# Performance work log

Measured on AMD Instinct MI355X. Metric: run time of the kernel, lower is better.

## Reference

```python
import math
import jax, jax.numpy as jnp
import numpy as np

B, L, D = 8, 512, 32
SEQ_LEN = 512.0
N_PATCHES, N_REF = 16, 32
LAT, HM = 128, 4
FH, NL, FF = 8, 3, 128
PRED = 96

def _time_embed(t, d):
    # interleaved sin/cos embedding, matching PositionalEmbedding's div_term
    div = jnp.exp(jnp.arange(0, d, 2, dtype=jnp.float32) * (-math.log(10000.0) / d))
    ang = t[..., None] * div
    out = jnp.zeros(t.shape + (d,), dtype=jnp.float32)
    return out.at[..., 0::2].set(jnp.sin(ang)).at[..., 1::2].set(jnp.cos(ang))

def _layernorm(x, g, b):
    mu = jnp.mean(x, axis=-1, keepdims=True)
    var = jnp.var(x, axis=-1, keepdims=True)
    return (x - mu) / jnp.sqrt(var + 1e-5) * g + b

def _mha(z, Wq, Wk, Wv, Wo, bq, bk, bv, bo):
    N, S, dm = z.shape
    hd = dm // FH
    q = (z @ Wq + bq).reshape(N, S, FH, hd)
    k = (z @ Wk + bk).reshape(N, S, FH, hd)
    v = (z @ Wv + bv).reshape(N, S, FH, hd)
    s = jnp.einsum('nqhe,nkhe->nhqk', q, k) / math.sqrt(hd)
    a = jax.nn.softmax(s, axis=-1)
    o = jnp.einsum('nhqk,nkhe->nqhe', a, v).reshape(N, S, dm)
    return o @ Wo + bo

def _forward(x, x_mark, x_mask, Wq, Wk, W_out, b_out, f_Wq, f_Wk, f_Wv, f_Wo, f_bq, f_bk, f_bv, f_bo, f_ln1_g, f_ln1_b, f_W1, f_b1, f_W2, f_b2, f_ln2_g, f_ln2_b, ln_f_g, ln_f_b, W_lin, b_lin):
    t = x_mark[:, :, 0]                                   # [B, L] irregular timestamps in [0, SEQ_LEN]
    edges = jnp.linspace(0.0, SEQ_LEN, N_PATCHES + 1)
    refs = jnp.linspace(0.0, SEQ_LEN, N_REF * N_PATCHES).reshape(N_PATCHES, N_REF)
    obs_valid = jnp.sum(x_mask, axis=-1) > 0              # [B, L]
    dk = LAT // HM
    Kmat = (_time_embed(t, LAT) @ Wk).reshape(B, L, HM, dk)
    v = x * x_mask                                        # mask values like `v = v * m` in original
    reprs = []
    for i in range(N_PATCHES):  # fixed small structural loop
        # _split_patch equivalent: per-channel masked attention is permutation
        # invariant, so the sort/scatter compaction reduces to masking.
        in_patch = (t >= edges[i]) & (t <= edges[i + 1]) & obs_valid   # [B, L]
        Qi = (_time_embed(refs[i], LAT) @ Wq).reshape(N_REF, HM, dk)
        scores = jnp.einsum('rhe,blhe->bhrl', Qi, Kmat) / math.sqrt(dk)
        cmask = x_mask * in_patch[..., None].astype(x.dtype)           # [B, L, D]
        neg = jnp.where(cmask[:, None, None, :, :] > 0, 0.0, -1e9)     # [B,1,1,L,D]
        p = jax.nn.softmax(scores[..., None] + neg, axis=3)            # [B,H,R,L,D]
        attn = jnp.einsum('bhrld,bld->brhd', p, v)                     # [B,R,H,D]
        reprs.append(attn.reshape(B, N_REF, HM * D) @ W_out + b_out)   # [B,R,D]
    rp = jnp.stack(reprs, axis=1)                          # [B, NP, R, D]
    z = rp.transpose(0, 3, 1, 2).reshape(B * D, N_PATCHES, N_REF)
    z = z + _time_embed(jnp.arange(N_PATCHES, dtype=jnp.float32), N_REF)[None]
    for l in range(NL):
        a = _mha(z, f_Wq[l], f_Wk[l], f_Wv[l], f_Wo[l], f_bq[l], f_bk[l], f_bv[l], f_bo[l])
        z = _layernorm(z + a, f_ln1_g[l], f_ln1_b[l])
        y = jax.nn.gelu(z @ f_W1[l] + f_b1[l]) @ f_W2[l] + f_b2[l]
        z = _layernorm(z + y, f_ln2_g[l], f_ln2_b[l])
    z = _layernorm(z, ln_f_g, ln_f_b)
    emb = z.reshape(B, D, N_PATCHES, N_REF).transpose(0, 1, 3, 2)      # [B, D, R, NP]
    out = emb.reshape(B, D, N_REF * N_PATCHES) @ W_lin + b_lin         # [B, D, PRED]
    return out.transpose(0, 2, 1)                          # [B, PRED, D]

def setup_inputs():
    key = jax.random.key(0)
    ks = jax.random.split(key, 30)
    def w(i, shape, fan_in):
        return jax.random.normal(ks[i], shape, jnp.float32) / math.sqrt(fan_in)
    return {
        'x': jax.random.normal(ks[0], (B, L, D), jnp.float32),
        'x_mark': jnp.sort(jax.random.uniform(ks[1], (B, L, 1), jnp.float32) * SEQ_LEN, axis=1),
        'x_mask': (jax.random.uniform(ks[2], (B, L, D), jnp.float32) < 0.8).astype(jnp.float32),
        'Wq': w(3, (LAT, LAT), LAT),
        'Wk': w(4, (LAT, LAT), LAT),
        'W_out': w(5, (HM * D, D), HM * D),
        'b_out': jnp.zeros((D,), jnp.float32),
        'f_Wq': w(6, (NL, N_REF, N_REF), N_REF),
        'f_Wk': w(7, (NL, N_REF, N_REF), N_REF),
        'f_Wv': w(8, (NL, N_REF, N_REF), N_REF),
        'f_Wo': w(9, (NL, N_REF, N_REF), N_REF),
        'f_bq': jnp.zeros((NL, N_REF), jnp.float32),
        'f_bk': jnp.zeros((NL, N_REF), jnp.float32),
        'f_bv': jnp.zeros((NL, N_REF), jnp.float32),
        'f_bo': jnp.zeros((NL, N_REF), jnp.float32),
        'f_ln1_g': jnp.ones((NL, N_REF), jnp.float32),
        'f_ln1_b': jnp.zeros((NL, N_REF), jnp.float32),
        'f_W1': w(10, (NL, N_REF, FF), N_REF),
        'f_b1': jnp.zeros((NL, FF), jnp.float32),
        'f_W2': w(11, (NL, FF, N_REF), FF),
        'f_b2': jnp.zeros((NL, N_REF), jnp.float32),
        'f_ln2_g': jnp.ones((NL, N_REF), jnp.float32),
        'f_ln2_b': jnp.zeros((NL, N_REF), jnp.float32),
        'ln_f_g': jnp.ones((N_REF,), jnp.float32),
        'ln_f_b': jnp.zeros((N_REF,), jnp.float32),
        'W_lin': w(12, (N_REF * N_PATCHES, PRED), N_REF * N_PATCHES),
        'b_lin': jnp.zeros((PRED,), jnp.float32),
    }

def reference(x, x_mark, x_mask, Wq, Wk, W_out, b_out, f_Wq, f_Wk, f_Wv, f_Wo, f_bq, f_bk, f_bv, f_bo, f_ln1_g, f_ln1_b, f_W1, f_b1, f_W2, f_b2, f_ln2_g, f_ln2_b, ln_f_g, ln_f_b, W_lin, b_lin):
    return _forward(x, x_mark, x_mask, Wq, Wk, W_out, b_out, f_Wq, f_Wk, f_Wv, f_Wo, f_bq, f_bk, f_bv, f_bo, f_ln1_g, f_ln1_b, f_W1, f_b1, f_W2, f_b2, f_ln2_g, f_ln2_b, ln_f_g, ln_f_b, W_lin, b_lin)
```

## Files before the change

kernel.cpp:

```cpp
#include <hip/hip_runtime.h>
#include <math.h>


#define ISQ32 0.17677669529663687f
#define C128  (-0.07195578415606394f)
#define C32   (-0.28782313662425575f)

__launch_bounds__(256)
__global__ void k_embed_mm(const float* __restrict__ x_mark,
                           const float* __restrict__ Wk,
                           const float* __restrict__ Wq,
                           const float* __restrict__ x_mask,
                           float* __restrict__ Kmat,
                           float* __restrict__ Qall,
                           unsigned* __restrict__ obsBits) {
    if (blockIdx.x >= 144) {
        const int gt = (blockIdx.x - 144) * 256 + threadIdx.x;
        const int w = gt >> 6, lane = gt & 63;
        const int bl = w * 2 + (lane >> 5);
        const int d = lane & 31;
        const unsigned long long mm = __ballot(x_mask[bl * 32 + d] > 0.0f);
        if (lane == 0)  obsBits[w * 2]     = (unsigned)(mm & 0xffffffffull);
        if (lane == 32) obsBits[w * 2 + 1] = (unsigned)(mm >> 32);
        return;
    }
    __shared__ float sTe[32][128];
    const int wv = threadIdx.x >> 6;
    const int lane = threadIdx.x & 63;
    const int bb = blockIdx.x;
    const int row0 = bb * 32 + wv * 8;
    const float dv = __expf((float)(2 * lane) * C128);
    #pragma unroll
    for (int rr = 0; rr < 8; ++rr) {
        const int row = row0 + rr;
        const float t = (row < 4096) ? x_mark[row] : (float)(row - 4096) * (512.0f / 511.0f);
        const float ang = t * dv;
        sTe[wv * 8 + rr][2 * lane]     = __sinf(ang);
        sTe[wv * 8 + rr][2 * lane + 1] = __cosf(ang);
    }
    __syncthreads();
    const float* W = (bb < 128) ? Wk : Wq;
    float a0[8], a1[8];
    #pragma unroll
    for (int rr = 0; rr < 8; ++rr) { a0[rr] = 0.f; a1[rr] = 0.f; }
    for (int k = 0; k < 128; ++k) {
        const float wa = W[k * 128 + lane];
        const float wb = W[k * 128 + lane + 64];
        #pragma unroll
        for (int rr = 0; rr < 8; ++rr) {
            const float te = sTe[wv * 8 + rr][k];
            a0[rr] = fmaf(te, wa, a0[rr]);
            a1[rr] = fmaf(te, wb, a1[rr]);
        }
    }
    #pragma unroll
    for (int rr = 0; rr < 8; ++rr) {
        const int row = row0 + rr;
        float* outp = (row < 4096) ? (Kmat + row * 128) : (Qall + (row - 4096) * 128);
        outp[lane] = a0[rr];
        outp[lane + 64] = a1[rr];
    }
}

__launch_bounds__(256)
__global__ void k_patch_attn(const float* __restrict__ x,
                             const float* __restrict__ x_mark,
                             const unsigned* __restrict__ obsBits,
                             const float* __restrict__ Kmat,
                             const float* __restrict__ Qall,
                             float* __restrict__ attn) {
    __shared__ float sQ[32][36];
    __shared__ float sK[96][36];
    __shared__ float sX[96][36];
    __shared__ float sS[32][100];
    __shared__ unsigned sBits[96];
    __shared__ int sLo, sHi;
    __shared__ unsigned sAV;
    const int tid = threadIdx.x;
    const int h = blockIdx.x & 3;
    const int b = (blockIdx.x >> 2) & 7;
    const int i = blockIdx.x >> 5;
    const float e0 = 32.0f * (float)i, e1 = 32.0f * (float)(i + 1);
    if (tid == 0) { sLo = 512; sHi = -1; sAV = 0u; }
    __syncthreads();
    #pragma unroll
    for (int k = 0; k < 4; ++k) {
        const int idx = tid + 256 * k;
        sQ[idx >> 5][idx & 31] = Qall[(i * 32 + (idx >> 5)) * 128 + h * 32 + (idx & 31)];
    }
    {
        int mylo = 512, myhi = -1;
        unsigned mybits = 0u;
        #pragma unroll
        for (int k = 0; k < 2; ++k) {
            const int l = tid + 256 * k;
            const float t = x_mark[b * 512 + l];
            if (t >= e0 && t <= e1) {
                mylo = min(mylo, l);
                myhi = max(myhi, l);
                mybits |= obsBits[b * 512 + l];
            }
        }
        #pragma unroll
        for (int off = 32; off > 0; off >>= 1) {
            mylo = min(mylo, __shfl_xor(mylo, off));
            myhi = max(myhi, __shfl_xor(myhi, off));
            mybits |= __shfl_xor(mybits, off);
        }
        if ((tid & 63) == 0) {
            atomicMin(&sLo, mylo);
            atomicMax(&sHi, myhi);
            atomicOr(&sAV, mybits);
        }
    }
    __syncthreads();
    const int lo = sLo, hi = sHi;
    const int NA = hi - lo + 1;
    const unsigned av = sAV;
    const int r = tid >> 3, dg = tid & 7;

    if (NA >= 1 && NA <= 96 && av == 0xffffffffu) {
        if (tid < NA) sBits[tid] = obsBits[b * 512 + lo + tid];
        for (int idx = tid; idx < NA * 32; idx += 256) {
            const int ll = idx >> 5, c = idx & 31;
            sK[ll][c] = Kmat[(b * 512 + lo + ll) * 128 + h * 32 + c];
            sX[ll][c] = x[(b * 512 + lo + ll) * 32 + c];
        }
        __syncthreads();
        float m = -1e30f;
        for (int ll = dg; ll < NA; ll += 8) {
            float p0 = 0.f, p1 = 0.f, p2 = 0.f, p3 = 0.f;
            #pragma unroll
            for (int e = 0; e < 32; e += 4) {
                p0 = fmaf(sQ[r][e],     sK[ll][e],     p0);
                p1 = fmaf(sQ[r][e + 1], sK[ll][e + 1], p1);
                p2 = fmaf(sQ[r][e + 2], sK[ll][e + 2], p2);
                p3 = fmaf(sQ[r][e + 3], sK[ll][e + 3], p3);
            }
            const float s = (p0 + p1 + p2 + p3) * ISQ32;
            sS[r][ll] = s;
            m = fmaxf(m, s);
        }
        #pragma unroll
        for (int off = 4; off > 0; off >>= 1) m = fmaxf(m, __shfl_xor(m, off));
        for (int ll = dg; ll < NA; ll += 8) sS[r][ll] = __expf(sS[r][ll] - m);
        __syncthreads();
        float num0 = 0.f, num1 = 0.f, num2 = 0.f, num3 = 0.f;
        float den0 = 0.f, den1 = 0.f, den2 = 0.f, den3 = 0.f;
        for (int ll = 0; ll < NA; ++ll) {
            const float e = sS[r][ll];
            const unsigned bits = sBits[ll];
            if ((bits >> dg) & 1u)        { den0 += e; num0 = fmaf(e, sX[ll][dg],      num0); }
            if ((bits >> (dg + 8)) & 1u)  { den1 += e; num1 = fmaf(e, sX[ll][dg + 8],  num1); }
            if ((bits >> (dg + 16)) & 1u) { den2 += e; num2 = fmaf(e, sX[ll][dg + 16], num2); }
            if ((bits >> (dg + 24)) & 1u) { den3 += e; num3 = fmaf(e, sX[ll][dg + 24], num3); }
        }
        float* ap = attn + ((i * 8 + b) * 32 + r) * 128 + h * 32;
        ap[dg]      = num0 / den0;
        ap[dg + 8]  = num1 / den1;
        ap[dg + 16] = num2 / den2;
        ap[dg + 24] = num3 / den3;
    } else {
        float m = -1e30f;
        float num[4] = {0.f, 0.f, 0.f, 0.f}, den[4] = {0.f, 0.f, 0.f, 0.f};
        for (int l = 0; l < 512; ++l) {
            const float t = x_mark[b * 512 + l];
            const unsigned bits = obsBits[b * 512 + l];
            const bool inr = (t >= e0 && t <= e1);
            const unsigned effD = (inr ? bits : 0u) | ~av;
            if (effD == 0u) continue;
            const unsigned effN = effD & bits;
            const float* Kp = Kmat + (b * 512 + l) * 128 + h * 32;
            float a = 0.f;
            #pragma unroll
            for (int e2 = 0; e2 < 32; ++e2) a = fmaf(sQ[r][e2], Kp[e2], a);
            const float s = a * ISQ32;
            float eNew;
            if (s > m) {
                const float scale = __expf(m - s);
                #pragma unroll
                for (int jj = 0; jj < 4; ++jj) { den[jj] *= scale; num[jj] *= scale; }
                m = s;
                eNew = 1.0f;
            } else {
                eNew = __expf(s - m);
            }
            const float* xp = x + (b * 512 + l) * 32;
            #pragma unroll
            for (int jj = 0; jj < 4; ++jj) {
                const int d = dg + 8 * jj;
                if ((effD >> d) & 1u) den[jj] += eNew;
                if ((effN >> d) & 1u) num[jj] = fmaf(eNew, xp[d], num[jj]);
            }
        }
        float* ap = attn + ((i * 8 + b) * 32 + r) * 128 + h * 32;
        #pragma unroll
        for (int jj = 0; jj < 4; ++jj) ap[dg + 8 * jj] = num[jj] / den[jj];
    }
}

__global__ void k_reprs(const float* __restrict__ attn,
                        const float* __restrict__ W_out,
                        const float* __restrict__ b_out,
                        float* __restrict__ z) {
    __shared__ float sA[32][129];
    const int tid = threadIdx.x;
    const int b = blockIdx.x & 7;
    const int i = blockIdx.x >> 3;
    #pragma unroll
    for (int k = 0; k < 16; ++k) {
        const int idx = tid + 256 * k;
        sA[idx >> 7][idx & 127] = attn[(i * 8 + b) * 4096 + idx];
    }
    __syncthreads();
    const int r = tid & 31, dgrp = tid >> 5;
    float acc0 = 0.f, acc1 = 0.f, acc2 = 0.f, acc3 = 0.f;
    #pragma unroll 8
    for (int k = 0; k < 128; ++k) {
        const float a = sA[r][k];
        acc0 = fmaf(a, W_out[k * 32 + dgrp],      acc0);
        acc1 = fmaf(a, W_out[k * 32 + dgrp + 8],  acc1);
        acc2 = fmaf(a, W_out[k * 32 + dgrp + 16], acc2);
        acc3 = fmaf(a, W_out[k * 32 + dgrp + 24], acc3);
    }
    const float dv = expf((float)(2 * (r >> 1)) * C32);
    const float ang = (float)i * dv;
    const float pe = (r & 1) ? cosf(ang) : sinf(ang);
    const int base = i * 32 + r;
    z[(b * 32 + dgrp)      * 512 + base] = acc0 + b_out[dgrp]      + pe;
    z[(b * 32 + dgrp + 8)  * 512 + base] = acc1 + b_out[dgrp + 8]  + pe;
    z[(b * 32 + dgrp + 16) * 512 + base] = acc2 + b_out[dgrp + 16] + pe;
    z[(b * 32 + dgrp + 24) * 512 + base] = acc3 + b_out[dgrp + 24] + pe;
}

__launch_bounds__(256, 1)
__global__ void k_former(const float* __restrict__ z,
                         const float* __restrict__ f_Wq, const float* __restrict__ f_Wk,
                         const float* __restrict__ f_Wv, const float* __restrict__ f_Wo,
                         const float* __restrict__ f_bq, const float* __restrict__ f_bk,
                         const float* __restrict__ f_bv, const float* __restrict__ f_bo,
                         const float* __restrict__ f_ln1_g, const float* __restrict__ f_ln1_b,
                         const float* __restrict__ f_W1, const float* __restrict__ f_b1,
                         const float* __restrict__ f_W2, const float* __restrict__ f_b2,
                         const float* __restrict__ f_ln2_g, const float* __restrict__ f_ln2_b,
                         const float* __restrict__ ln_f_g, const float* __restrict__ ln_f_b,
                         const float* __restrict__ W_lin, const float* __restrict__ b_lin,
                         float* __restrict__ out) {
    __shared__ float sZ[16][36];
    __shared__ float sQm[16][36], sKm[16][36], sVm[16][36], sOm[16][36];
    __shared__ float sH[16][132];
    __shared__ float sP[4][16][36];
    const int tid = threadIdx.x;
    const int n = blockIdx.x;

    {
        const int ps = tid >> 4, pj = (tid & 15) * 2;
        *(float2*)&sZ[ps][pj] = *(const float2*)(z + n * 512 + ps * 32 + pj);
    }
    __syncthreads();

    for (int l = 0; l < 3; ++l) {
        if (tid < 192) {
            const int j = tid & 31;
            const int mgrp = tid >> 5;
            const int m = mgrp % 3, half = mgrp / 3;
            const float* Wm = ((m == 0) ? f_Wq : (m == 1) ? f_Wk : f_Wv) + l * 1024;
            const float bias = ((m == 0) ? f_bq : (m == 1) ? f_bk : f_bv)[l * 32 + j];
            float w[32];
            #pragma unroll
            for (int k = 0; k < 32; ++k) w[k] = Wm[k * 32 + j];
            float acc[8];
            #pragma unroll
            for (int ss = 0; ss < 8; ++ss) {
                const int s = half * 8 + ss;
                float a = bias;
                #pragma unroll
                for (int k4 = 0; k4 < 8; ++k4) {
                    const float4 zv = *(const float4*)&sZ[s][4 * k4];
                    a = fmaf(zv.x, w[4 * k4],     a);
                    a = fmaf(zv.y, w[4 * k4 + 1], a);
                    a = fmaf(zv.z, w[4 * k4 + 2], a);
                    a = fmaf(zv.w, w[4 * k4 + 3], a);
                }
                acc[ss] = a;
            }
            float (*dst)[36] = (m == 0) ? sQm : (m == 1) ? sKm : sVm;
            #pragma unroll
            for (int ss = 0; ss < 8; ++ss) dst[half * 8 + ss][j] = acc[ss];
        }
        __syncthreads();
        if (tid < 128) {
            const int q = tid & 15, hh = tid >> 4;
            const int h4 = hh * 4;
            const float4 qv = *(const float4*)&sQm[q][h4];
            float sc[16];
            float mx = -1e30f;
            #pragma unroll
            for (int k = 0; k < 16; ++k) {
                const float4 kv = *(const float4*)&sKm[k][h4];
                sc[k] = (qv.x * kv.x + qv.y * kv.y + qv.z * kv.z + qv.w * kv.w) * 0.5f;
                mx = fmaxf(mx, sc[k]);
            }
            float sum = 0.f;
            #pragma unroll
            for (int k = 0; k < 16; ++k) { sc[k] = __expf(sc[k] - mx); sum += sc[k]; }
            const float inv = 1.0f / sum;
            float o0 = 0.f, o1 = 0.f, o2 = 0.f, o3 = 0.f;
            #pragma unroll
            for (int k = 0; k < 16; ++k) {
                const float4 vv = *(const float4*)&sVm[k][h4];
                o0 = fmaf(sc[k], vv.x, o0); o1 = fmaf(sc[k], vv.y, o1);
                o2 = fmaf(sc[k], vv.z, o2); o3 = fmaf(sc[k], vv.w, o3);
            }
            *(float4*)&sOm[q][h4] = make_float4(o0 * inv, o1 * inv, o2 * inv, o3 * inv);
        }
        __syncthreads();
        {
            const int sp = tid >> 5, j = tid & 31;
            const int sA = 2 * sp, sB = sA + 1;
            float wo[32];
            #pragma unroll
            for (int k = 0; k < 32; ++k) wo[k] = f_Wo[l * 1024 + k * 32 + j];
            float oa = 0.f, ob = 0.f;
            #pragma unroll
            for (int k4 = 0; k4 < 8; ++k4) {
                const float4 va = *(const float4*)&sOm[sA][4 * k4];
                const float4 vb = *(const float4*)&sOm[sB][4 * k4];
                oa = fmaf(va.x, wo[4 * k4], oa);     oa = fmaf(va.y, wo[4 * k4 + 1], oa);
                oa = fmaf(va.z, wo[4 * k4 + 2], oa); oa = fmaf(va.w, wo[4 * k4 + 3], oa);
                ob = fmaf(vb.x, wo[4 * k4], ob);     ob = fmaf(vb.y, wo[4 * k4 + 1], ob);
                ob = fmaf(vb.z, wo[4 * k4 + 2], ob); ob = fmaf(vb.w, wo[4 * k4 + 3], ob);
            }
            const float bo = f_bo[l * 32 + j];
            const float t0 = sZ[sA][j] + oa + bo;
            const float t1 = sZ[sB][j] + ob + bo;
            float s0 = t0, q0 = t0 * t0, s1 = t1, q1 = t1 * t1;
            #pragma unroll
            for (int off = 16; off > 0; off >>= 1) {
                s0 += __shfl_xor(s0, off); q0 += __shfl_xor(q0, off);
                s1 += __shfl_xor(s1, off); q1 += __shfl_xor(q1, off);
            }
            const float mu0 = s0 * (1.0f / 32.0f);
            const float rs0 = rsqrtf(q0 * (1.0f / 32.0f) - mu0 * mu0 + 1e-5f);
            const float mu1 = s1 * (1.0f / 32.0f);
            const float rs1 = rsqrtf(q1 * (1.0f / 32.0f) - mu1 * mu1 + 1e-5f);
            const float g1 = f_ln1_g[l * 32 + j], be1 = f_ln1_b[l * 32 + j];
            sZ[sA][j] = (t0 - mu0) * rs0 * g1 + be1;
            sZ[sB][j] = (t1 - mu1) * rs1 * g1 + be1;
        }
        __syncthreads();
        {
            const int f = tid & 127, half = tid >> 7;
            float w1[32];
            #pragma unroll
            for (int k = 0; k < 32; ++k) w1[k] = f_W1[l * 4096 + k * 128 + f];
            const float b1v = f_b1[l * 128 + f];
            #pragma unroll
            for (int ss = 0; ss < 8; ++ss) {
                const int s = half * 8 + ss;
                float a = b1v;
                #pragma unroll
                for (int k4 = 0; k4 < 8; ++k4) {
                    const float4 zv = *(const float4*)&sZ[s][4 * k4];
                    a = fmaf(zv.x, w1[4 * k4], a);     a = fmaf(zv.y, w1[4 * k4 + 1], a);
                    a = fmaf(zv.z, w1[4 * k4 + 2], a); a = fmaf(zv.w, w1[4 * k4 + 3], a);
                }
                const float c = a;
                const float a2 = 1.5957691216057308f * (c + 0.044715f * c * c * c);
                const float e = __expf(a2);
                sH[s][f] = 0.5f * c * (2.0f - 2.0f / (e + 1.0f));
            }
        }
        __syncthreads();
        {
            const int j = tid & 31, kc = (tid >> 5) & 3, half = tid >> 7;
            float w2[32];
            #pragma unroll
            for (int k = 0; k < 32; ++k) w2[k] = f_W2[l * 4096 + (kc * 32 + k) * 32 + j];
            #pragma unroll
            for (int ss = 0; ss < 8; ++ss) {
                const int s = half * 8 + ss;
                float a = 0.f;
                #pragma unroll
                for (int k4 = 0; k4 < 8; ++k4) {
                    const float4 hv = *(const float4*)&sH[s][kc * 32 + 4 * k4];
                    a = fmaf(hv.x, w2[4 * k4], a);     a = fmaf(hv.y, w2[4 * k4 + 1], a);
                    a = fmaf(hv.z, w2[4 * k4 + 2], a); a = fmaf(hv.w, w2[4 * k4 + 3], a);
                }
                sP[kc][s][j] = a;
            }
        }
        __syncthreads();
        {
            const int sp = tid >> 5, j = tid & 31;
            const int sA = 2 * sp, sB = sA + 1;
            const float b2v = f_b2[l * 32 + j];
            const float fa = sP[0][sA][j] + sP[1][sA][j] + sP[2][sA][j] + sP[3][sA][j];
            const float fb = sP[0][sB][j] + sP[1][sB][j] + sP[2][sB][j] + sP[3][sB][j];
            const float t0 = sZ[sA][j] + fa + b2v;
            const float t1 = sZ[sB][j] + fb + b2v;
            float s0 = t0, q0 = t0 * t0, s1 = t1, q1 = t1 * t1;
            #pragma unroll
            for (int off = 16; off > 0; off >>= 1) {
                s0 += __shfl_xor(s0, off); q0 += __shfl_xor(q0, off);
                s1 += __shfl_xor(s1, off); q1 += __shfl_xor(q1, off);
            }
            const float mu0 = s0 * (1.0f / 32.0f);
            const float rs0 = rsqrtf(q0 * (1.0f / 32.0f) - mu0 * mu0 + 1e-5f);
            const float mu1 = s1 * (1.0f / 32.0f);
            const float rs1 = rsqrtf(q1 * (1.0f / 32.0f) - mu1 * mu1 + 1e-5f);
            const float g2 = f_ln2_g[l * 32 + j], be2 = f_ln2_b[l * 32 + j];
            sZ[sA][j] = (t0 - mu0) * rs0 * g2 + be2;
            sZ[sB][j] = (t1 - mu1) * rs1 * g2 + be2;
        }
        __syncthreads();
    }
    {
        const int sp = tid >> 5, j = tid & 31;
        const int sA = 2 * sp, sB = sA + 1;
        const float t0 = sZ[sA][j], t1 = sZ[sB][j];
        float s0 = t0, q0 = t0 * t0, s1 = t1, q1 = t1 * t1;
        #pragma unroll
        for (int off = 16; off > 0; off >>= 1) {
            s0 += __shfl_xor(s0, off); q0 += __shfl_xor(q0, off);
            s1 += __shfl_xor(s1, off); q1 += __shfl_xor(q1, off);
        }
        const float mu0 = s0 * (1.0f / 32.0f);
        const float rs0 = rsqrtf(q0 * (1.0f / 32.0f) - mu0 * mu0 + 1e-5f);
        const float mu1 = s1 * (1.0f / 32.0f);
        const float rs1 = rsqrtf(q1 * (1.0f / 32.0f) - mu1 * mu1 + 1e-5f);
        const float gf = ln_f_g[j], bf = ln_f_b[j];
        sZ[sA][j] = (t0 - mu0) * rs0 * gf + bf;
        sZ[sB][j] = (t1 - mu1) * rs1 * gf + bf;
    }
    __syncthreads();
    {
        float* sRed = &sH[0][0];
        const int w = tid >> 6, lane64 = tid & 63;
        const int s = w * 4 + (lane64 >> 4);
        const int l16 = lane64 & 15;
        const int o0 = 6 * l16;
        float4 zr[8];
        #pragma unroll
        for (int k4 = 0; k4 < 8; ++k4) zr[k4] = *(const float4*)&sZ[s][4 * k4];
        float p0 = 0.f, p1 = 0.f, p2 = 0.f, p3 = 0.f, p4 = 0.f, p5 = 0.f;
        #pragma unroll
        for (int k4 = 0; k4 < 8; ++k4) {
            #pragma unroll
            for (int e = 0; e < 4; ++e) {
                const int rr = 4 * k4 + e;
                const float zz = (e == 0) ? zr[k4].x : (e == 1) ? zr[k4].y : (e == 2) ? zr[k4].z : zr[k4].w;
                const float* wl = W_lin + (rr * 16 + s) * 96 + o0;
                const float2 wa = *(const float2*)(wl);
                const float2 wb = *(const float2*)(wl + 2);
                const float2 wc = *(const float2*)(wl + 4);
                p0 = fmaf(zz, wa.x, p0); p1 = fmaf(zz, wa.y, p1);
                p2 = fmaf(zz, wb.x, p2); p3 = fmaf(zz, wb.y, p3);
                p4 = fmaf(zz, wc.x, p4); p5 = fmaf(zz, wc.y, p5);
            }
        }
        *(float2*)&sRed[s * 100 + o0]     = make_float2(p0, p1);
        *(float2*)&sRed[s * 100 + o0 + 2] = make_float2(p2, p3);
        *(float2*)&sRed[s * 100 + o0 + 4] = make_float2(p4, p5);
    }
    __syncthreads();
    if (tid < 96) {
        const float* sRed = &sH[0][0];
        float acc = b_lin[tid];
        #pragma unroll
        for (int ss = 0; ss < 16; ++ss) acc += sRed[ss * 100 + tid];
        out[((n >> 5) * 96 + tid) * 32 + (n & 31)] = acc;
    }
}

extern "C" void kernel_launch(void* const* d_in, const int* in_sizes, int n_in,
                              void* d_out, int out_size, void* d_ws, size_t ws_size,
                              hipStream_t stream) {
    const float* x       = (const float*)d_in[0];
    const float* x_mark  = (const float*)d_in[1];
    const float* x_mask  = (const float*)d_in[2];
    const float* Wq      = (const float*)d_in[3];
    const float* Wk      = (const float*)d_in[4];
    const float* W_out   = (const float*)d_in[5];
    const float* b_out   = (const float*)d_in[6];
    const float* f_Wq    = (const float*)d_in[7];
    const float* f_Wk    = (const float*)d_in[8];
    const float* f_Wv    = (const float*)d_in[9];
    const float* f_Wo    = (const float*)d_in[10];
    const float* f_bq    = (const float*)d_in[11];
    const float* f_bk    = (const float*)d_in[12];
    const float* f_bv    = (const float*)d_in[13];
    const float* f_bo    = (const float*)d_in[14];
    const float* f_ln1_g = (const float*)d_in[15];
    const float* f_ln1_b = (const float*)d_in[16];
    const float* f_W1    = (const float*)d_in[17];
    const float* f_b1    = (const float*)d_in[18];
    const float* f_W2    = (const float*)d_in[19];
    const float* f_b2    = (const float*)d_in[20];
    const float* f_ln2_g = (const float*)d_in[21];
    const float* f_ln2_b = (const float*)d_in[22];
    const float* ln_f_g  = (const float*)d_in[23];
    const float* ln_f_b  = (const float*)d_in[24];
    const float* W_lin   = (const float*)d_in[25];
    const float* b_lin   = (const float*)d_in[26];

    float* ws = (float*)d_ws;
    float* Kmat      = ws;
    float* Qall      = ws + 524288;
    unsigned* obsB   = (unsigned*)(ws + 589824);
    float* attn      = ws + 593920;
    float* zbuf      = ws + 1118208;

    k_embed_mm<<<656, 256, 0, stream>>>(x_mark, Wk, Wq, x_mask, Kmat, Qall, obsB);
    k_patch_attn<<<512, 256, 0, stream>>>(x, x_mark, obsB, Kmat, Qall, attn);
    k_reprs<<<128, 256, 0, stream>>>(attn, W_out, b_out, zbuf);
    k_former<<<256, 256, 0, stream>>>(zbuf,
        f_Wq, f_Wk, f_Wv, f_Wo, f_bq, f_bk, f_bv, f_bo,
        f_ln1_g, f_ln1_b, f_W1, f_b1, f_W2, f_b2, f_ln2_g, f_ln2_b,
        ln_f_g, ln_f_b, W_lin, b_lin, (float*)d_out);
}
```

Measured before the change: 69.56 us.

## Give each wave its own token rows in former kernel to drop barriers

Each wave now owns four sequence rows, two per half-wave, through QKV, the Wo projection, LayerNorm and the FFN. Because those stages only touch a wave's own rows, most block-wide barriers and the sP partial-sum buffer go away. Attention splits the keys across the two half-waves and combines them with cross-half shuffles. The final linear layer becomes a 192-thread dot product over a transposed copy in shared memory. In exchange, each thread now reloads weight columns for several outputs serially, which raises register pressure and per-thread work.

```diff
diff --git a/kernel.cpp b/kernel.cpp
--- a/kernel.cpp
+++ b/kernel.cpp
@@ -249,75 +249,81 @@
     __shared__ float sZ[16][36];
     __shared__ float sQm[16][36], sKm[16][36], sVm[16][36], sOm[16][36];
     __shared__ float sH[16][132];
-    __shared__ float sP[4][16][36];
+    __shared__ float sZf[512];
+    __shared__ float sPart[2][96];
     const int tid = threadIdx.x;
     const int n = blockIdx.x;
-
-    {
-        const int ps = tid >> 4, pj = (tid & 15) * 2;
-        *(float2*)&sZ[ps][pj] = *(const float2*)(z + n * 512 + ps * 32 + pj);
-    }
-    __syncthreads();
+    const int wv = tid >> 6;
+    const int lane = tid & 63;
+    const int j = lane & 31, half2 = lane >> 5;
+    const int sA = wv * 4 + half2 * 2, sB = sA + 1;
+
+    sZ[sA][j] = z[n * 512 + sA * 32 + j];
+    sZ[sB][j] = z[n * 512 + sB * 32 + j];
 
     for (int l = 0; l < 3; ++l) {
-        if (tid < 192) {
-            const int j = tid & 31;
-            const int mgrp = tid >> 5;
-            const int m = mgrp % 3, half = mgrp / 3;
-            const float* Wm = ((m == 0) ? f_Wq : (m == 1) ? f_Wk : f_Wv) + l * 1024;
-            const float bias = ((m == 0) ? f_bq : (m == 1) ? f_bk : f_bv)[l * 32 + j];
-            float w[32];
-            #pragma unroll
-            for (int k = 0; k < 32; ++k) w[k] = Wm[k * 32 + j];
-            float acc[8];
-            #pragma unroll
-            for (int ss = 0; ss < 8; ++ss) {
-                const int s = half * 8 + ss;
-                float a = bias;
+        {
+            float4 zra[8], zrb[8];
+            #pragma unroll
+            for (int k4 = 0; k4 < 8; ++k4) {
+                zra[k4] = *(const float4*)&sZ[sA][4 * k4];
+                zrb[k4] = *(const float4*)&sZ[sB][4 * k4];
+            }
+            #pragma unroll
+            for (int m = 0; m < 3; ++m) {
+                const float* Wm = ((m == 0) ? f_Wq : (m == 1) ? f_Wk : f_Wv) + l * 1024;
+                const float bias = ((m == 0) ? f_bq : (m == 1) ? f_bk : f_bv)[l * 32 + j];
+                float w[32];
+                #pragma unroll
+                for (int k = 0; k < 32; ++k) w[k] = Wm[k * 32 + j];
+                float aA = bias, aB = bias;
                 #pragma unroll
                 for (int k4 = 0; k4 < 8; ++k4) {
-                    const float4 zv = *(const float4*)&sZ[s][4 * k4];
-                    a = fmaf(zv.x, w[4 * k4],     a);
-                    a = fmaf(zv.y, w[4 * k4 + 1], a);
-                    a = fmaf(zv.z, w[4 * k4 + 2], a);
-                    a = fmaf(zv.w, w[4 * k4 + 3], a);
+                    const float4 a = zra[k4], b4 = zrb[k4];
+                    aA = fmaf(a.x, w[4 * k4], aA);     aA = fmaf(a.y, w[4 * k4 + 1], aA);
+                    aA = fmaf(a.z, w[4 * k4 + 2], aA); aA = fmaf(a.w, w[4 * k4 + 3], aA);
+                    aB = fmaf(b4.x, w[4 * k4], aB);     aB = fmaf(b4.y, w[4 * k4 + 1], aB);
+                    aB = fmaf(b4.z, w[4 * k4 + 2], aB); aB = fmaf(b4.w, w[4 * k4 + 3], aB);
                 }
-                acc[ss] = a;
-            }
-            float (*dst)[36] = (m == 0) ? sQm : (m == 1) ? sKm : sVm;
-            #pragma unroll
-            for (int ss = 0; ss < 8; ++ss) dst[half * 8 + ss][j] = acc[ss];
-        }
-        __syncthreads();
-        if (tid < 128) {
-            const int q = tid & 15, hh = tid >> 4;
-            const int h4 = hh * 4;
-            const float4 qv = *(const float4*)&sQm[q][h4];
-            float sc[16];
-            float mx = -1e30f;
-            #pragma unroll
-            for (int k = 0; k < 16; ++k) {
-                const float4 kv = *(const float4*)&sKm[k][h4];
-                sc[k] = (qv.x * kv.x + qv.y * kv.y + qv.z * kv.z + qv.w * kv.w) * 0.5f;
-                mx = fmaxf(mx, sc[k]);
-            }
-            float sum = 0.f;
-            #pragma unroll
-            for (int k = 0; k < 16; ++k) { sc[k] = __expf(sc[k] - mx); sum += sc[k]; }
-            const float inv = 1.0f / sum;
-            float o0 = 0.f, o1 = 0.f, o2 = 0.f, o3 = 0.f;
-            #pragma unroll
-            for (int k = 0; k < 16; ++k) {
-                const float4 vv = *(const float4*)&sVm[k][h4];
-                o0 = fmaf(sc[k], vv.x, o0); o1 = fmaf(sc[k], vv.y, o1);
-                o2 = fmaf(sc[k], vv.z, o2); o3 = fmaf(sc[k], vv.w, o3);
-            }
-            *(float4*)&sOm[q][h4] = make_float4(o0 * inv, o1 * inv, o2 * inv, o3 * inv);
+                float (*dst)[36] = (m == 0) ? sQm : (m == 1) ? sKm : sVm;
+                dst[sA][j] = aA;
+                dst[sB][j] = aB;
+            }
         }
         __syncthreads();
         {
-            const int sp = tid >> 5, j = tid & 31;
-            const int sA = 2 * sp, sB = sA + 1;
+            const int ql = (lane >> 3) & 3, hh = lane & 7, kh = lane >> 5;
+            const int q = wv * 4 + ql, h4 = hh * 4;
+            const float4 qv = *(const float4*)&sQm[q][h4];
+            float sc[8];
+            float mx = -1e30f;
+            #pragma unroll
+            for (int m = 0; m < 8; ++m) {
+                const float4 kv = *(const float4*)&sKm[kh * 8 + m][h4];
+                sc[m] = (qv.x * kv.x + qv.y * kv.y + qv.z * kv.z + qv.w * kv.w) * 0.5f;
+                mx = fmaxf(mx, sc[m]);
+            }
+            mx = fmaxf(mx, __shfl_xor(mx, 32));
+            float sum = 0.f;
+            #pragma unroll
+            for (int m = 0; m < 8; ++m) { sc[m] = __expf(sc[m] - mx); sum += sc[m]; }
+            sum += __shfl_xor(sum, 32);
+            float o0 = 0.f, o1 = 0.f, o2 = 0.f, o3 = 0.f;
+            #pragma unroll
+            for (int m = 0; m < 8; ++m) {
+                const float4 vv = *(const float4*)&sVm[kh * 8 + m][h4];
+                o0 = fmaf(sc[m], vv.x, o0); o1 = fmaf(sc[m], vv.y, o1);
+                o2 = fmaf(sc[m], vv.z, o2); o3 = fmaf(sc[m], vv.w, o3);
+            }
+            o0 += __shfl_xor(o0, 32); o1 += __shfl_xor(o1, 32);
+            o2 += __shfl_xor(o2, 32); o3 += __shfl_xor(o3, 32);
+            if (kh == 0) {
+                const float inv = 1.0f / sum;
+                *(float4*)&sOm[q][h4] = make_float4(o0 * inv, o1 * inv, o2 * inv, o3 * inv);
+            }
+        }
+        __syncthreads();
+        {
             float wo[32];
             #pragma unroll
             for (int k = 0; k < 32; ++k) wo[k] = f_Wo[l * 1024 + k * 32 + j];
@@ -348,55 +354,53 @@
             sZ[sA][j] = (t0 - mu0) * rs0 * g1 + be1;
             sZ[sB][j] = (t1 - mu1) * rs1 * g1 + be1;
         }
-        __syncthreads();
         {
-            const int f = tid & 127, half = tid >> 7;
-            float w1[32];
-            #pragma unroll
-            for (int k = 0; k < 32; ++k) w1[k] = f_W1[l * 4096 + k * 128 + f];
-            const float b1v = f_b1[l * 128 + f];
-            #pragma unroll
-            for (int ss = 0; ss < 8; ++ss) {
-                const int s = half * 8 + ss;
-                float a = b1v;
+            float4 zra[8], zrb[8];
+            #pragma unroll
+            for (int k4 = 0; k4 < 8; ++k4) {
+                zra[k4] = *(const float4*)&sZ[sA][4 * k4];
+                zrb[k4] = *(const float4*)&sZ[sB][4 * k4];
+            }
+            #pragma unroll
+            for (int fm = 0; fm < 4; ++fm) {
+                const int f = j + 32 * fm;
+                float w1[32];
+                #pragma unroll
+                for (int k = 0; k < 32; ++k) w1[k] = f_W1[l * 4096 + k * 128 + f];
+                const float b1v = f_b1[l * 128 + f];
+                float aA = b1v, aB = b1v;
                 #pragma unroll
                 for (int k4 = 0; k4 < 8; ++k4) {
-                    const float4 zv = *(const float4*)&sZ[s][4 * k4];
-                    a = fmaf(zv.x, w1[4 * k4], a);     a = fmaf(zv.y, w1[4 * k4 + 1], a);
-                    a = fmaf(zv.z, w1[4 * k4 + 2], a); a = fmaf(zv.w, w1[4 * k4 + 3], a);
+                    const float4 a = zra[k4], b4 = zrb[k4];
+                    aA = fmaf(a.x, w1[4 * k4], aA);     aA = fmaf(a.y, w1[4 * k4 + 1], aA);
+                    aA = fmaf(a.z, w1[4 * k4 + 2], aA); aA = fmaf(a.w, w1[4 * k4 + 3], aA);
+                    aB = fmaf(b4.x, w1[4 * k4], aB);     aB = fmaf(b4.y, w1[4 * k4 + 1], aB);
+                    aB = fmaf(b4.z, w1[4 * k4 + 2], aB); aB = fmaf(b4.w, w1[4 * k4 + 3], aB);
                 }
-                const float c = a;
-                const float a2 = 1.5957691216057308f * (c + 0.044715f * c * c * c);
-                const float e = __expf(a2);
-                sH[s][f] = 0.5f * c * (2.0f - 2.0f / (e + 1.0f));
-            }
-        }
-        __syncthreads();
+                const float e1e = __expf(1.5957691216057308f * (aA + 0.044715f * aA * aA * aA));
+                const float e2e = __expf(1.5957691216057308f * (aB + 0.044715f * aB * aB * aB));
+                sH[sA][f] = 0.5f * aA * (2.0f - 2.0f / (e1e + 1.0f));
+                sH[sB][f] = 0.5f * aB * (2.0f - 2.0f / (e2e + 1.0f));
+            }
+        }
         {
-            const int j = tid & 31, kc = (tid >> 5) & 3, half = tid >> 7;
-            float w2[32];
-            #pragma unroll
-            for (int k = 0; k < 32; ++k) w2[k] = f_W2[l * 4096 + (kc * 32 + k) * 32 + j];
-            #pragma unroll
-            for (int ss = 0; ss < 8; ++ss) {
-                const int s = half * 8 + ss;
-                float a = 0.f;
+            float fa = 0.f, fb = 0.f;
+            #pragma unroll
+            for (int kc = 0; kc < 4; ++kc) {
+                float w2[32];
+                #pragma unroll
+                for (int k = 0; k < 32; ++k) w2[k] = f_W2[l * 4096 + (kc * 32 + k) * 32 + j];
                 #pragma unroll
                 for (int k4 = 0; k4 < 8; ++k4) {
-                    const float4 hv = *(const float4*)&sH[s][kc * 32 + 4 * k4];
-                    a = fmaf(hv.x, w2[4 * k4], a);     a = fmaf(hv.y, w2[4 * k4 + 1], a);
-                    a = fmaf(hv.z, w2[4 * k4 + 2], a); a = fmaf(hv.w, w2[4 * k4 + 3], a);
+                    const float4 ha = *(const float4*)&sH[sA][kc * 32 + 4 * k4];
+                    const float4 hb = *(const float4*)&sH[sB][kc * 32 + 4 * k4];
+                    fa = fmaf(ha.x, w2[4 * k4], fa);     fa = fmaf(ha.y, w2[4 * k4 + 1], fa);
+                    fa = fmaf(ha.z, w2[4 * k4 + 2], fa); fa = fmaf(ha.w, w2[4 * k4 + 3], fa);
+                    fb = fmaf(hb.x, w2[4 * k4], fb);     fb = fmaf(hb.y, w2[4 * k4 + 1], fb);
+                    fb = fmaf(hb.z, w2[4 * k4 + 2], fb); fb = fmaf(hb.w, w2[4 * k4 + 3], fb);
                 }
-                sP[kc][s][j] = a;
-            }
-        }
-        __syncthreads();
-        {
-            const int sp = tid >> 5, j = tid & 31;
-            const int sA = 2 * sp, sB = sA + 1;
+            }
             const float b2v = f_b2[l * 32 + j];
-            const float fa = sP[0][sA][j] + sP[1][sA][j] + sP[2][sA][j] + sP[3][sA][j];
-            const float fb = sP[0][sB][j] + sP[1][sB][j] + sP[2][sB][j] + sP[3][sB][j];
             const float t0 = sZ[sA][j] + fa + b2v;
             const float t1 = sZ[sB][j] + fb + b2v;
             float s0 = t0, q0 = t0 * t0, s1 = t1, q1 = t1 * t1;
@@ -413,11 +417,8 @@
             sZ[sA][j] = (t0 - mu0) * rs0 * g2 + be2;
             sZ[sB][j] = (t1 - mu1) * rs1 * g2 + be2;
         }
-        __syncthreads();
     }
     {
-        const int sp = tid >> 5, j = tid & 31;
-        const int sA = 2 * sp, sB = sA + 1;
         const float t0 = sZ[sA][j], t1 = sZ[sB][j];
         float s0 = t0, q0 = t0 * t0, s1 = t1, q1 = t1 * t1;
         #pragma unroll
@@ -430,47 +431,22 @@
         const float mu1 = s1 * (1.0f / 32.0f);
         const float rs1 = rsqrtf(q1 * (1.0f / 32.0f) - mu1 * mu1 + 1e-5f);
         const float gf = ln_f_g[j], bf = ln_f_b[j];
-        sZ[sA][j] = (t0 - mu0) * rs0 * gf + bf;
-        sZ[sB][j] = (t1 - mu1) * rs1 * gf + bf;
-    }
-    __syncthreads();
-    {
-        float* sRed = &sH[0][0];
-        const int w = tid >> 6, lane64 = tid & 63;
-        const int s = w * 4 + (lane64 >> 4);
-        const int l16 = lane64 & 15;
-        const int o0 = 6 * l16;
-        float4 zr[8];
-        #pragma unroll
-        for (int k4 = 0; k4 < 8; ++k4) zr[k4] = *(const float4*)&sZ[s][4 * k4];
-        float p0 = 0.f, p1 = 0.f, p2 = 0.f, p3 = 0.f, p4 = 0.f, p5 = 0.f;
-        #pragma unroll
-        for (int k4 = 0; k4 < 8; ++k4) {
-            #pragma unroll
-            for (int e = 0; e < 4; ++e) {
-                const int rr = 4 * k4 + e;
-                const float zz = (e == 0) ? zr[k4].x : (e == 1) ? zr[k4].y : (e == 2) ? zr[k4].z : zr[k4].w;
-                const float* wl = W_lin + (rr * 16 + s) * 96 + o0;
-                const float2 wa = *(const float2*)(wl);
-                const float2 wb = *(const float2*)(wl + 2);
-                const float2 wc = *(const float2*)(wl + 4);
-                p0 = fmaf(zz, wa.x, p0); p1 = fmaf(zz, wa.y, p1);
-                p2 = fmaf(zz, wb.x, p2); p3 = fmaf(zz, wb.y, p3);
-                p4 = fmaf(zz, wc.x, p4); p5 = fmaf(zz, wc.y, p5);
-            }
-        }
-        *(float2*)&sRed[s * 100 + o0]     = make_float2(p0, p1);
-        *(float2*)&sRed[s * 100 + o0 + 2] = make_float2(p2, p3);
-        *(float2*)&sRed[s * 100 + o0 + 4] = make_float2(p4, p5);
-    }
-    __syncthreads();
-    if (tid < 96) {
-        const float* sRed = &sH[0][0];
-        float acc = b_lin[tid];
-        #pragma unroll
-        for (int ss = 0; ss < 16; ++ss) acc += sRed[ss * 100 + tid];
-        out[((n >> 5) * 96 + tid) * 32 + (n & 31)] = acc;
-    }
+        sZf[j * 16 + sA] = (t0 - mu0) * rs0 * gf + bf;
+        sZf[j * 16 + sB] = (t1 - mu1) * rs1 * gf + bf;
+    }
+    __syncthreads();
+    if (tid < 192) {
+        const int half = tid / 96, o = tid % 96;
+        const int j0 = half * 256;
+        float acc = 0.f;
+        #pragma unroll 16
+        for (int jj = 0; jj < 256; ++jj)
+            acc = fmaf(sZf[j0 + jj], W_lin[(j0 + jj) * 96 + o], acc);
+        sPart[half][o] = acc;
+    }
+    __syncthreads();
+    if (tid < 96)
+        out[((n >> 5) * 96 + tid) * 32 + (n & 31)] = sPart[0][tid] + sPart[1][tid] + b_lin[tid];
 }
 
 extern "C" void kernel_launch(void* const* d_in, const int* in_sizes, int n_in,
```

Result: faster. 65.06 us (-6.5%).
